# Performance work log

Measured on AMD Instinct MI355X. Metric: run time of the kernel, lower is better.

The kernel has to match this reference:

```python
import jax, jax.numpy as jnp
import numpy as np

N = 100000
E = 1600000
NFEAT = 256
NCLASS = 40
H1, C1 = 8, 8  # layer1: 8 heads x 8 channels, concat -> 64
EPS = 1e-16
NEG_SLOPE = 0.2


def setup_inputs() -> dict:
    key = jax.random.key(0)
    ks = jax.random.split(key, 10)
    x = jax.random.normal(ks[0], (N, NFEAT), dtype=jnp.float32)
    # random edges with no self-loops (PyG GATConv removes then re-adds self loops)
    src = jax.random.randint(ks[1], (E,), 0, N)
    off = jax.random.randint(ks[2], (E,), 1, N)
    dst = (src + off) % N
    edge_index = jnp.stack([src, dst]).astype(jnp.int64)
    glorot = lambda k, shp, fan: jax.random.uniform(k, shp, jnp.float32, -1.0, 1.0) * np.sqrt(6.0 / fan)
    # layer 1: in=256 -> heads=8, out=8
    W1 = glorot(ks[3], (NFEAT, H1 * C1), NFEAT + H1 * C1)
    att_src1 = glorot(ks[4], (H1, C1), 2 * C1)
    att_dst1 = glorot(ks[5], (H1, C1), 2 * C1)
    b1 = jnp.zeros((H1 * C1,), jnp.float32)
    # layer 2: in=64 -> heads=1, out=nclass
    W2 = glorot(ks[6], (H1 * C1, NCLASS), H1 * C1 + NCLASS)
    att_src2 = glorot(ks[7], (1, NCLASS), 2 * NCLASS)
    att_dst2 = glorot(ks[8], (1, NCLASS), 2 * NCLASS)
    b2 = jnp.zeros((NCLASS,), jnp.float32)
    return {"x": x, "edge_index": edge_index, "W1": W1, "att_src1": att_src1,
            "att_dst1": att_dst1, "b1": b1, "W2": W2, "att_src2": att_src2,
            "att_dst2": att_dst2, "b2": b2}


def gat_conv(x, src, dst, W, att_src, att_dst, bias, heads, out_ch):
    n = x.shape[0]
    h = (x @ W).reshape(n, heads, out_ch)               # [N,H,C]
    a_src = (h * att_src[None]).sum(-1)                  # [N,H]
    a_dst = (h * att_dst[None]).sum(-1)                  # [N,H]
    e = jax.nn.leaky_relu(a_src[src] + a_dst[dst], NEG_SLOPE)  # [E,H]
    # segment softmax over incoming edges of each target node
    m = jax.ops.segment_max(e, dst, num_segments=n)
    e = jnp.exp(e - m[dst])
    s = jax.ops.segment_sum(e, dst, num_segments=n)
    alpha = e / (s[dst] + EPS)                           # [E,H]
    msg = h[src] * alpha[..., None]                      # [E,H,C]
    out = jax.ops.segment_sum(msg, dst, num_segments=n)  # [N,H,C]
    return out.reshape(n, heads * out_ch) + bias


def reference(x, edge_index, W1, att_src1, att_dst1, b1, W2, att_src2, att_dst2, b2):
    # add self loops (PyG GATConv default add_self_loops=True)
    loops = jnp.arange(N, dtype=edge_index.dtype)
    src = jnp.concatenate([edge_index[0], loops])
    dst = jnp.concatenate([edge_index[1], loops])
    h = gat_conv(x, src, dst, W1, att_src1, att_dst1, b1, H1, C1)  # [N,64]
    h = jax.nn.elu(h)
    out = gat_conv(h, src, dst, W2, att_src2, att_dst2, b2, 1, NCLASS)  # [N,nclass]
    return out
```

## Files before the change

kernel.cpp:

```cpp
#include <hip/hip_runtime.h>
#include <hip/hip_bf16.h>

#define NN 100000
#define NE 1600000
#define NF 256
#define NC 40
#define NH 8
#define D1 64
#define NEG 0.2f
#define BSHIFT 7
#define BSZ 128
#define NB ((NN + BSZ - 1) / BSZ)
#define EPB 4096
#define NBLK ((NE + EPB - 1) / EPB)

typedef __attribute__((ext_vector_type(8))) short short8;
typedef __attribute__((ext_vector_type(4))) float f32x4;

static __device__ __forceinline__ float lrelu(float x) { return x > 0.f ? x : NEG * x; }

static __device__ __forceinline__ float2 bfx2(unsigned u) {
    union { unsigned q; float f; } a, b;
    a.q = u << 16;
    b.q = u & 0xFFFF0000u;
    return make_float2(a.f, b.f);
}

static __device__ __forceinline__ unsigned packbf2(float x, float y) {
    unsigned xu = __float_as_uint(x), yu = __float_as_uint(y);
    xu = (xu + 0x7FFFu + ((xu >> 16) & 1u)) >> 16;
    yu = (yu + 0x7FFFu + ((yu >> 16) & 1u)) >> 16;
    return xu | (yu << 16);
}

static __device__ __forceinline__ unsigned short f2b(float x) {
    unsigned u = __float_as_uint(x);
    u = (u + 0x7FFFu + ((u >> 16) & 1u)) >> 16;
    return (unsigned short)u;
}


__launch_bounds__(256)
__global__ void bhist_k(const int* __restrict__ dst, int* __restrict__ cnt) {
    __shared__ int hist[NB];
    int i = blockIdx.x, t = threadIdx.x;
    for (int b = t; b < NB; b += 256) hist[b] = 0;
    __syncthreads();
    int e0 = i * EPB;
    #pragma unroll
    for (int k = 0; k < EPB / 256; ++k) {
        int e = e0 + k * 256 + t;
        if (e < NE) atomicAdd(&hist[dst[e] >> BSHIFT], 1);
    }
    __syncthreads();
    for (int b = t; b < NB; b += 256) cnt[i * NB + b] = hist[b];
}

__launch_bounds__(256)
__global__ void bscan2_k(int* __restrict__ cnt, int* __restrict__ btot) {
    __shared__ int ps[256];
    int b = blockIdx.x, t = threadIdx.x;
    int i0 = 2 * t;
    int a = (i0 < NBLK) ? cnt[i0 * NB + b] : 0;
    int c = (i0 + 1 < NBLK) ? cnt[(i0 + 1) * NB + b] : 0;
    int s = a + c;
    ps[t] = s;
    __syncthreads();
    #pragma unroll
    for (int off = 1; off < 256; off <<= 1) {
        int x = (t >= off) ? ps[t - off] : 0;
        __syncthreads();
        ps[t] += x;
        __syncthreads();
    }
    int ex = ps[t] - s;
    if (i0 < NBLK) cnt[i0 * NB + b] = ex;
    if (i0 + 1 < NBLK) cnt[(i0 + 1) * NB + b] = ex + a;
    if (t == 255) btot[b] = ps[255];
}

__launch_bounds__(256)
__global__ void bscanB_k(const int* __restrict__ btot, int* __restrict__ bbase) {
    __shared__ int ps[256];
    int t = threadIdx.x;
    int j0 = 4 * t;
    int v[4]; int s = 0;
    #pragma unroll
    for (int k = 0; k < 4; ++k) { v[k] = (j0 + k < NB) ? btot[j0 + k] : 0; s += v[k]; }
    ps[t] = s;
    __syncthreads();
    #pragma unroll
    for (int off = 1; off < 256; off <<= 1) {
        int x = (t >= off) ? ps[t - off] : 0;
        __syncthreads();
        ps[t] += x;
        __syncthreads();
    }
    int run = ps[t] - s;
    #pragma unroll
    for (int k = 0; k < 4; ++k) { if (j0 + k < NB) bbase[j0 + k] = run; run += v[k]; }
    if (t == 0) bbase[NB] = NE;
}

__launch_bounds__(256)
__global__ void bplace_k(const int* __restrict__ src, const int* __restrict__ dst,
                         const int* __restrict__ cnt, const int* __restrict__ bbase,
                         unsigned* __restrict__ tmp) {
    __shared__ int loff[NB];
    int i = blockIdx.x, t = threadIdx.x;
    for (int b = t; b < NB; b += 256) loff[b] = bbase[b] + cnt[i * NB + b];
    __syncthreads();
    int e0 = i * EPB;
    #pragma unroll
    for (int k = 0; k < EPB / 256; ++k) {
        int e = e0 + k * 256 + t;
        if (e < NE) {
            int d = dst[e];
            int p = atomicAdd(&loff[d >> BSHIFT], 1);
            tmp[p] = ((unsigned)(d & 127) << 17) | (unsigned)src[e];
        }
    }
}

__launch_bounds__(256)
__global__ void scatter2_k(const unsigned* __restrict__ tmp, const int* __restrict__ bbase,
                           int* __restrict__ rowptr, int* __restrict__ col) {
    __shared__ int lcnt[BSZ];
    __shared__ int lrow[BSZ];
    __shared__ int ls[BSZ];
    int b = blockIdx.x, t = threadIdx.x;
    int n0 = b << BSHIFT;
    if (t < BSZ) lcnt[t] = 0;
    __syncthreads();
    int beg = bbase[b], end = bbase[b + 1];
    for (int p = beg + t; p < end; p += 256)
        atomicAdd(&lcnt[tmp[p] >> 17], 1);
    __syncthreads();
    if (t < BSZ) ls[t] = lcnt[t];
    __syncthreads();
    #pragma unroll
    for (int off = 1; off < BSZ; off <<= 1) {
        int x = 0;
        if (t < BSZ && t >= off) x = ls[t - off];
        __syncthreads();
        if (t < BSZ) ls[t] += x;
        __syncthreads();
    }
    if (t < BSZ) {
        int ex = ls[t] - lcnt[t];
        lrow[t] = beg + ex;
        if (n0 + t < NN) rowptr[n0 + t] = beg + ex;
        lcnt[t] = 0;
    }
    if (b == NB - 1 && t == 0) rowptr[NN] = NE;
    __syncthreads();
    for (int p = beg + t; p < end; p += 256) {
        unsigned v = tmp[p];
        int dloc = v >> 17;
        int s = (int)(v & 0x1FFFFu);
        int o = atomicAdd(&lcnt[dloc], 1);
        col[lrow[dloc] + o] = s;
    }
}


__launch_bounds__(256)
__global__ void gemm1_k(const float* __restrict__ x, const float* __restrict__ W,
                        unsigned short* __restrict__ h1b) {
    __shared__ unsigned short wsw[8 * 4 * 64 * 8];
    int tid = threadIdx.x;
    int wid = tid >> 6, lane = tid & 63;
    int r0 = blockIdx.x * 128 + wid * 32;

    #pragma unroll
    for (int it = 0; it < 16; ++it) {
        int idx4 = it * 256 + tid;
        int k = idx4 >> 4;
        int c0 = (idx4 & 15) * 4;
        float4 v = *(const float4*)&W[k * 64 + c0];
        int kt = k >> 5, kg = (k >> 3) & 3, kr = k & 7;
        float vv[4] = {v.x, v.y, v.z, v.w};
        #pragma unroll
        for (int j = 0; j < 4; ++j) {
            int c = c0 + j;
            int dest = (((kt * 4 + (c >> 4)) * 64) + kg * 16 + (c & 15)) * 8 + kr;
            wsw[dest] = f2b(vv[j]);
        }
    }
    __syncthreads();

    int arow0 = r0 + (lane & 15);
    int kg8 = (lane >> 4) * 8;
    f32x4 acc[2][4] = {};
    for (int kt = 0; kt < 8; ++kt) {
        short8 af[2];
        #pragma unroll
        for (int rt = 0; rt < 2; ++rt) {
            int row = arow0 + rt * 16;
            float4 v0 = make_float4(0.f, 0.f, 0.f, 0.f), v1 = v0;
            if (row < NN) {
                const float* px = &x[row * NF + kt * 32 + kg8];
                v0 = *(const float4*)px;
                v1 = *(const float4*)(px + 4);
            }
            unsigned p0 = packbf2(v0.x, v0.y), p1 = packbf2(v0.z, v0.w);
            unsigned p2 = packbf2(v1.x, v1.y), p3 = packbf2(v1.z, v1.w);
            af[rt][0] = (short)(p0 & 0xFFFF); af[rt][1] = (short)(p0 >> 16);
            af[rt][2] = (short)(p1 & 0xFFFF); af[rt][3] = (short)(p1 >> 16);
            af[rt][4] = (short)(p2 & 0xFFFF); af[rt][5] = (short)(p2 >> 16);
            af[rt][6] = (short)(p3 & 0xFFFF); af[rt][7] = (short)(p3 >> 16);
        }
        #pragma unroll
        for (int ct = 0; ct < 4; ++ct) {
            short8 bf = *(const short8*)&wsw[((kt * 4 + ct) * 64 + lane) * 8];
            acc[0][ct] = __builtin_amdgcn_mfma_f32_16x16x32_bf16(af[0], bf, acc[0][ct], 0, 0, 0);
            acc[1][ct] = __builtin_amdgcn_mfma_f32_16x16x32_bf16(af[1], bf, acc[1][ct], 0, 0, 0);
        }
    }

    int ccol = lane & 15;
    int crow0 = r0 + (lane >> 4) * 4;
    #pragma unroll
    for (int rt = 0; rt < 2; ++rt) {
        #pragma unroll
        for (int r = 0; r < 4; ++r) {
            int grow = crow0 + rt * 16 + r;
            if (grow < NN) {
                #pragma unroll
                for (int ct = 0; ct < 4; ++ct)
                    h1b[grow * D1 + ct * 16 + ccol] = f2b(acc[rt][ct][r]);
            }
        }
    }
}


__global__ void attn1_k(const unsigned short* __restrict__ h1b, const float* __restrict__ asrc,
                        const float* __restrict__ adst,
                        float* __restrict__ as1, float* __restrict__ ad1) {
    int t = blockIdx.x * blockDim.x + threadIdx.x;
    if (t >= NN * NH) return;
    int n = t >> 3, h = t & 7;
    uint4 v = *(const uint4*)&h1b[n * D1 + h * 8];
    float hv[8];
    float2 p;
    p = bfx2(v.x); hv[0] = p.x; hv[1] = p.y;
    p = bfx2(v.y); hv[2] = p.x; hv[3] = p.y;
    p = bfx2(v.z); hv[4] = p.x; hv[5] = p.y;
    p = bfx2(v.w); hv[6] = p.x; hv[7] = p.y;
    float sa = 0.f, sd = 0.f;
    #pragma unroll
    for (int c = 0; c < 8; ++c) {
        sa = fmaf(hv[c], asrc[h * 8 + c], sa);
        sd = fmaf(hv[c], adst[h * 8 + c], sd);
    }
    as1[t] = sa;
    ad1[t] = sd;
}


__launch_bounds__(128)
__global__ void w2pre_k(const float* __restrict__ W2, const float* __restrict__ asrc,
                        const float* __restrict__ adst, float* __restrict__ w2vec) {
    int t = threadIdx.x;
    int c = t & 63;
    const float* av = (t < 64) ? asrc : adst;
    float s = 0.f;
    #pragma unroll
    for (int j = 0; j < NC; ++j) s = fmaf(W2[c * NC + j], av[j], s);
    w2vec[t] = s;
}


__launch_bounds__(256)
__global__ void agg1_k(const unsigned short* __restrict__ h1b, const float* __restrict__ as1,
                       const float* __restrict__ ad1,
                       const int* __restrict__ rowptr, const int* __restrict__ col,
                       const float* __restrict__ b1, const float* __restrict__ w2vec,
                       unsigned short* __restrict__ h1outb,
                       float* __restrict__ as2, float* __restrict__ ad2) {
    int n = blockIdx.x * 4 + (threadIdx.x >> 6);
    if (n >= NN) return;
    int lane = threadIdx.x & 63;
    int g = lane >> 3, ln = lane & 7;
    int row0 = rowptr[n];
    int d = rowptr[n + 1] - row0;
    float adh = ad1[n * 8 + ln];

    float acc[8] = {};
    float wsum = 0.f;
    for (int j = 0; j <= d; j += 8) {
        int jj = j + g;
        int s = (jj < d) ? col[row0 + jj] : n;
        float e = lrelu(as1[s * 8 + ln] + adh);
        float wgt = (jj <= d) ? __expf(e) : 0.f;
        wsum += wgt;
        uint4 hv = *(const uint4*)&h1b[s * D1 + ln * 8];
        float2 p;
        p = bfx2(hv.x); acc[0] = fmaf(p.x, wgt, acc[0]); acc[1] = fmaf(p.y, wgt, acc[1]);
        p = bfx2(hv.y); acc[2] = fmaf(p.x, wgt, acc[2]); acc[3] = fmaf(p.y, wgt, acc[3]);
        p = bfx2(hv.z); acc[4] = fmaf(p.x, wgt, acc[4]); acc[5] = fmaf(p.y, wgt, acc[5]);
        p = bfx2(hv.w); acc[6] = fmaf(p.x, wgt, acc[6]); acc[7] = fmaf(p.y, wgt, acc[7]);
    }
    #pragma unroll
    for (int off = 8; off <= 32; off <<= 1) {
        wsum += __shfl_xor(wsum, off, 64);
        #pragma unroll
        for (int k = 0; k < 8; ++k) acc[k] += __shfl_xor(acc[k], off, 64);
    }
    if (g == 0) {
        float inv = 1.f / (wsum + 1e-16f);
        float vals[8];
        #pragma unroll
        for (int k = 0; k < 8; ++k) {
            float v = fmaf(acc[k], inv, b1[ln * 8 + k]);
            vals[k] = (v > 0.f) ? v : (__expf(v) - 1.f);
        }
        unsigned u[4];
        #pragma unroll
        for (int k = 0; k < 4; ++k) u[k] = packbf2(vals[2 * k], vals[2 * k + 1]);
        uint4 w = {u[0], u[1], u[2], u[3]};
        *(uint4*)&h1outb[n * D1 + ln * 8] = w;
        float pa = 0.f, pd = 0.f;
        #pragma unroll
        for (int k = 0; k < 8; ++k) {
            pa = fmaf(vals[k], w2vec[ln * 8 + k], pa);
            pd = fmaf(vals[k], w2vec[64 + ln * 8 + k], pd);
        }
        pa += __shfl_xor(pa, 1); pa += __shfl_xor(pa, 2); pa += __shfl_xor(pa, 4);
        pd += __shfl_xor(pd, 1); pd += __shfl_xor(pd, 2); pd += __shfl_xor(pd, 4);
        if (ln == 0) { as2[n] = pa; ad2[n] = pd; }
    }
}


__launch_bounds__(256)
__global__ void agg2_k(const unsigned short* __restrict__ h1outb, const float* __restrict__ as2,
                       const float* __restrict__ ad2,
                       const int* __restrict__ rowptr, const int* __restrict__ col,
                       unsigned short* __restrict__ zb) {
    int n = blockIdx.x * 4 + (threadIdx.x >> 6);
    if (n >= NN) return;
    int lane = threadIdx.x & 63;
    int g = lane >> 3, ln = lane & 7;
    int row0 = rowptr[n];
    int d = rowptr[n + 1] - row0;
    float adn = ad2[n];

    float acc[8] = {};
    float wsum = 0.f;
    for (int j = 0; j <= d; j += 8) {
        int jj = j + g;
        int s = (jj < d) ? col[row0 + jj] : n;
        float e = lrelu(as2[s] + adn);
        float wgt = (jj <= d) ? __expf(e) : 0.f;
        wsum += wgt;
        uint4 hv = *(const uint4*)&h1outb[s * D1 + ln * 8];
        float2 p;
        p = bfx2(hv.x); acc[0] = fmaf(p.x, wgt, acc[0]); acc[1] = fmaf(p.y, wgt, acc[1]);
        p = bfx2(hv.y); acc[2] = fmaf(p.x, wgt, acc[2]); acc[3] = fmaf(p.y, wgt, acc[3]);
        p = bfx2(hv.z); acc[4] = fmaf(p.x, wgt, acc[4]); acc[5] = fmaf(p.y, wgt, acc[5]);
        p = bfx2(hv.w); acc[6] = fmaf(p.x, wgt, acc[6]); acc[7] = fmaf(p.y, wgt, acc[7]);
    }
    #pragma unroll
    for (int off = 8; off <= 32; off <<= 1) {
        wsum += __shfl_xor(wsum, off, 64);
        #pragma unroll
        for (int k = 0; k < 8; ++k) acc[k] += __shfl_xor(acc[k], off, 64);
    }
    if (g == 0) {
        float inv = 1.f / (wsum + 1e-16f);
        unsigned u[4];
        #pragma unroll
        for (int k = 0; k < 4; ++k)
            u[k] = packbf2(acc[2 * k] * inv, acc[2 * k + 1] * inv);
        uint4 w = {u[0], u[1], u[2], u[3]};
        *(uint4*)&zb[n * D1 + ln * 8] = w;
    }
}


__launch_bounds__(256)
__global__ void gemm2_k(const unsigned short* __restrict__ zb, const float* __restrict__ W2,
                        const float* __restrict__ b2, float* __restrict__ out) {
    __shared__ float xs[64 * 68];
    __shared__ float wsm[64 * 40];
    __shared__ float bs[40];
    int r0 = blockIdx.x * 64;
    int tid = threadIdx.x;
    #pragma unroll
    for (int it = 0; it < 4; ++it) {
        int idx = tid + it * 256;
        int row = idx >> 4;
        int q = (idx & 15) * 4;
        int gr = r0 + row;
        float f0 = 0.f, f1 = 0.f, f2 = 0.f, f3 = 0.f;
        if (gr < NN) {
            uint2 v = *(const uint2*)&zb[gr * D1 + q];
            float2 p0 = bfx2(v.x), p1 = bfx2(v.y);
            f0 = p0.x; f1 = p0.y; f2 = p1.x; f3 = p1.y;
        }
        xs[row * 68 + q] = f0;
        xs[row * 68 + q + 1] = f1;
        xs[row * 68 + q + 2] = f2;
        xs[row * 68 + q + 3] = f3;
    }
    #pragma unroll
    for (int it = 0; it < 10; ++it) {
        int idx = tid + it * 256;
        if (idx < 64 * 40) wsm[idx] = W2[idx];
    }
    if (tid < 40) bs[tid] = b2[tid];
    __syncthreads();
    int r = tid >> 2, q = tid & 3;
    float acc[10] = {};
    #pragma unroll 4
    for (int k = 0; k < 64; ++k) {
        float xv = xs[r * 68 + k];
        #pragma unroll
        for (int i = 0; i < 10; ++i)
            acc[i] = fmaf(xv, wsm[k * 40 + q * 10 + i], acc[i]);
    }
    int gr = r0 + r;
    if (gr < NN) {
        #pragma unroll
        for (int i = 0; i < 10; ++i) out[gr * NC + q * 10 + i] = acc[i] + bs[q * 10 + i];
    }
}


extern "C" void kernel_launch(void* const* d_in, const int* in_sizes, int n_in,
                              void* d_out, int out_size, void* d_ws, size_t ws_size,
                              hipStream_t stream) {
    const float* x = (const float*)d_in[0];
    const int* ei = (const int*)d_in[1];
    const int* src = ei;
    const int* dst = ei + NE;
    const float* W1 = (const float*)d_in[2];
    const float* asrc1 = (const float*)d_in[3];
    const float* adst1 = (const float*)d_in[4];
    const float* b1 = (const float*)d_in[5];
    const float* W2 = (const float*)d_in[6];
    const float* asrc2 = (const float*)d_in[7];
    const float* adst2 = (const float*)d_in[8];
    const float* b2 = (const float*)d_in[9];
    float* out = (float*)d_out;

    char* ws = (char*)d_ws;
    unsigned short* h1b    = (unsigned short*)(ws + 0);
    unsigned short* zb     = (unsigned short*)(ws + 0);
    float*          as1    = (float*)(ws + 12800000);
    float*          ad1    = (float*)(ws + 16000000);
    unsigned short* h1outb = (unsigned short*)(ws + 25600000);
    unsigned*       tmp    = (unsigned*)(ws + 25600000);
    float*          as2    = (float*)(ws + 38400000);
    float*          ad2    = (float*)(ws + 38800000);
    int*            col    = (int*)(ws + 39200000);
    int*            cnt    = (int*)(ws + 39200000);
    int*            rowptr = (int*)(ws + 45600000);
    int*            btot   = (int*)(ws + 46000128);
    int*            bbase  = (int*)(ws + 46003264);
    float*          w2vec  = (float*)(ws + 46006400);

    bhist_k<<<NBLK, 256, 0, stream>>>(dst, cnt);
    bscan2_k<<<NB, 256, 0, stream>>>(cnt, btot);
    bscanB_k<<<1, 256, 0, stream>>>(btot, bbase);
    bplace_k<<<NBLK, 256, 0, stream>>>(src, dst, cnt, bbase, tmp);
    scatter2_k<<<NB, 256, 0, stream>>>(tmp, bbase, rowptr, col);

    gemm1_k<<<(NN + 127) / 128, 256, 0, stream>>>(x, W1, h1b);
    attn1_k<<<(NN * NH + 255) / 256, 256, 0, stream>>>(h1b, asrc1, adst1, as1, ad1);
    w2pre_k<<<1, 128, 0, stream>>>(W2, asrc2, adst2, w2vec);
    agg1_k<<<(NN + 3) / 4, 256, 0, stream>>>(h1b, as1, ad1, rowptr, col, b1, w2vec,
                                             h1outb, as2, ad2);

    agg2_k<<<(NN + 3) / 4, 256, 0, stream>>>(h1outb, as2, ad2, rowptr, col, zb);
    gemm2_k<<<(NN + 63) / 64, 256, 0, stream>>>(zb, W2, b2, out);
}
```

Baseline: 212.0 us.

## Fuse attention scores into GEMM epilogue and recompute source scores in aggregation

Drops the separate attn1 kernel. The destination attention score is now computed in the gemm1 epilogue using a shuffle reduction over the MFMA output columns. The source score is recomputed per edge inside agg1 from the gathered h1 row, which agg1 already loads. This removes a kernel launch, one read pass over h1b and the as1 buffer with its random gathers, in exchange for extra FMAs per edge and shuffles in the GEMM epilogue.

```diff
diff --git a/kernel.cpp b/kernel.cpp
--- a/kernel.cpp
+++ b/kernel.cpp
@@ -166,7 +166,8 @@
 
 __launch_bounds__(256)
 __global__ void gemm1_k(const float* __restrict__ x, const float* __restrict__ W,
-                        unsigned short* __restrict__ h1b) {
+                        const float* __restrict__ adst1,
+                        unsigned short* __restrict__ h1b, float* __restrict__ ad1) {
     __shared__ unsigned short wsw[8 * 4 * 64 * 8];
     int tid = threadIdx.x;
     int wid = tid >> 6, lane = tid & 63;
@@ -220,6 +221,11 @@
 
     int ccol = lane & 15;
     int crow0 = r0 + (lane >> 4) * 4;
+    float adc[4];
+    #pragma unroll
+    for (int ct = 0; ct < 4; ++ct) adc[ct] = adst1[ct * 16 + ccol];
+    int hbase = ccol >> 3;
+
     #pragma unroll
     for (int rt = 0; rt < 2; ++rt) {
         #pragma unroll
@@ -230,32 +236,20 @@
                 for (int ct = 0; ct < 4; ++ct)
                     h1b[grow * D1 + ct * 16 + ccol] = f2b(acc[rt][ct][r]);
             }
-        }
-    }
-}
-
-
-__global__ void attn1_k(const unsigned short* __restrict__ h1b, const float* __restrict__ asrc,
-                        const float* __restrict__ adst,
-                        float* __restrict__ as1, float* __restrict__ ad1) {
-    int t = blockIdx.x * blockDim.x + threadIdx.x;
-    if (t >= NN * NH) return;
-    int n = t >> 3, h = t & 7;
-    uint4 v = *(const uint4*)&h1b[n * D1 + h * 8];
-    float hv[8];
-    float2 p;
-    p = bfx2(v.x); hv[0] = p.x; hv[1] = p.y;
-    p = bfx2(v.y); hv[2] = p.x; hv[3] = p.y;
-    p = bfx2(v.z); hv[4] = p.x; hv[5] = p.y;
-    p = bfx2(v.w); hv[6] = p.x; hv[7] = p.y;
-    float sa = 0.f, sd = 0.f;
-    #pragma unroll
-    for (int c = 0; c < 8; ++c) {
-        sa = fmaf(hv[c], asrc[h * 8 + c], sa);
-        sd = fmaf(hv[c], adst[h * 8 + c], sd);
-    }
-    as1[t] = sa;
-    ad1[t] = sd;
+            float pd[4];
+            #pragma unroll
+            for (int ct = 0; ct < 4; ++ct) pd[ct] = acc[rt][ct][r] * adc[ct];
+            #pragma unroll
+            for (int off = 1; off <= 4; off <<= 1)
+                #pragma unroll
+                for (int ct = 0; ct < 4; ++ct) pd[ct] += __shfl_xor(pd[ct], off, 64);
+            if ((lane & 7) == 0 && grow < NN) {
+                #pragma unroll
+                for (int ct = 0; ct < 4; ++ct)
+                    ad1[grow * 8 + ct * 2 + hbase] = pd[ct];
+            }
+        }
+    }
 }
 
 
@@ -273,7 +267,7 @@
 
 
 __launch_bounds__(256)
-__global__ void agg1_k(const unsigned short* __restrict__ h1b, const float* __restrict__ as1,
+__global__ void agg1_k(const unsigned short* __restrict__ h1b, const float* __restrict__ asrc1,
                        const float* __restrict__ ad1,
                        const int* __restrict__ rowptr, const int* __restrict__ col,
                        const float* __restrict__ b1, const float* __restrict__ w2vec,
@@ -286,21 +280,29 @@
     int row0 = rowptr[n];
     int d = rowptr[n + 1] - row0;
     float adh = ad1[n * 8 + ln];
+    float a1c[8];
+    #pragma unroll
+    for (int k = 0; k < 8; ++k) a1c[k] = asrc1[ln * 8 + k];
 
     float acc[8] = {};
     float wsum = 0.f;
     for (int j = 0; j <= d; j += 8) {
         int jj = j + g;
         int s = (jj < d) ? col[row0 + jj] : n;
-        float e = lrelu(as1[s * 8 + ln] + adh);
-        float wgt = (jj <= d) ? __expf(e) : 0.f;
+        uint4 hv = *(const uint4*)&h1b[s * D1 + ln * 8];
+        float f[8];
+        float2 p;
+        p = bfx2(hv.x); f[0] = p.x; f[1] = p.y;
+        p = bfx2(hv.y); f[2] = p.x; f[3] = p.y;
+        p = bfx2(hv.z); f[4] = p.x; f[5] = p.y;
+        p = bfx2(hv.w); f[6] = p.x; f[7] = p.y;
+        float sa = 0.f;
+        #pragma unroll
+        for (int k = 0; k < 8; ++k) sa = fmaf(f[k], a1c[k], sa);
+        float wgt = (jj <= d) ? __expf(lrelu(sa + adh)) : 0.f;
         wsum += wgt;
-        uint4 hv = *(const uint4*)&h1b[s * D1 + ln * 8];
-        float2 p;
-        p = bfx2(hv.x); acc[0] = fmaf(p.x, wgt, acc[0]); acc[1] = fmaf(p.y, wgt, acc[1]);
-        p = bfx2(hv.y); acc[2] = fmaf(p.x, wgt, acc[2]); acc[3] = fmaf(p.y, wgt, acc[3]);
-        p = bfx2(hv.z); acc[4] = fmaf(p.x, wgt, acc[4]); acc[5] = fmaf(p.y, wgt, acc[5]);
-        p = bfx2(hv.w); acc[6] = fmaf(p.x, wgt, acc[6]); acc[7] = fmaf(p.y, wgt, acc[7]);
+        #pragma unroll
+        for (int k = 0; k < 8; ++k) acc[k] = fmaf(f[k], wgt, acc[k]);
     }
     #pragma unroll
     for (int off = 8; off <= 32; off <<= 1) {
@@ -449,7 +451,6 @@
     char* ws = (char*)d_ws;
     unsigned short* h1b    = (unsigned short*)(ws + 0);
     unsigned short* zb     = (unsigned short*)(ws + 0);
-    float*          as1    = (float*)(ws + 12800000);
     float*          ad1    = (float*)(ws + 16000000);
     unsigned short* h1outb = (unsigned short*)(ws + 25600000);
     unsigned*       tmp    = (unsigned*)(ws + 25600000);
@@ -468,10 +469,9 @@
     bplace_k<<<NBLK, 256, 0, stream>>>(src, dst, cnt, bbase, tmp);
     scatter2_k<<<NB, 256, 0, stream>>>(tmp, bbase, rowptr, col);
 
-    gemm1_k<<<(NN + 127) / 128, 256, 0, stream>>>(x, W1, h1b);
-    attn1_k<<<(NN * NH + 255) / 256, 256, 0, stream>>>(h1b, asrc1, adst1, as1, ad1);
+    gemm1_k<<<(NN + 127) / 128, 256, 0, stream>>>(x, W1, adst1, h1b, ad1);
     w2pre_k<<<1, 128, 0, stream>>>(W2, asrc2, adst2, w2vec);
-    agg1_k<<<(NN + 3) / 4, 256, 0, stream>>>(h1b, as1, ad1, rowptr, col, b1, w2vec,
+    agg1_k<<<(NN + 3) / 4, 256, 0, stream>>>(h1b, asrc1, ad1, rowptr, col, b1, w2vec,
                                              h1outb, as2, ad2);
 
     agg2_k<<<(NN + 3) / 4, 256, 0, stream>>>(h1outb, as2, ad2, rowptr, col, zb);
```

Result: no change. 208.7 us (-1.6%).
